# Performance work log

Hardware: AMD Instinct MI355X
Metric: run time of the kernel (lower is better)

Reference implementation:

```python
import jax, jax.numpy as jnp
import numpy as np

N_CTX = 4096
D_MODEL = 2048


def setup_inputs() -> dict:
    key = jax.random.key(0)
    k1, k2, k3 = jax.random.split(key, 3)
    embedding = jax.random.normal(k1, (N_CTX, D_MODEL), dtype=jnp.float32)
    # torch.rand -> uniform [0, 1)
    qk = jax.random.uniform(k2, (D_MODEL, D_MODEL), dtype=jnp.float32)
    ov = jax.random.uniform(k3, (D_MODEL, D_MODEL), dtype=jnp.float32)
    return {"embedding": embedding, "qk": qk, "ov": ov}


def reference(embedding, qk, ov):
    n = embedding.shape[0]
    # scores[i, j] = e_i @ qk @ e_j  -> [N, N]
    scores = (embedding @ qk) @ embedding.T
    # strict upper triangle gets -inf (causal mask), matching triu(-inf, diag=1)
    causal_mask = jnp.triu(jnp.full((n, n), -jnp.inf, dtype=scores.dtype), k=1)
    scores = scores + causal_mask
    attn = jax.nn.softmax(scores, axis=-1)  # nn.Softmax() on 2D -> dim=1
    return (attn @ embedding) @ ov
```

## Files before the change

### kernel.cpp

```cpp
#include <hip/hip_runtime.h>
#include <hip/hip_bf16.h>

#define N_CTX 4096
#define DM    2048

typedef __attribute__((ext_vector_type(8))) short short8;
typedef __attribute__((ext_vector_type(4))) float f32x4;
typedef unsigned short ushort_t;

__device__ __forceinline__ ushort_t f2bf(float x) {
    __hip_bfloat16 h = __float2bfloat16(x);
    return __builtin_bit_cast(ushort_t, h);
}
__device__ __forceinline__ float bf2f(ushort_t u) {
    return __bfloat162float(__builtin_bit_cast(__hip_bfloat16, u));
}

__device__ __forceinline__ void gload16(const void* g, void* l) {
    __builtin_amdgcn_global_load_lds((const __attribute__((address_space(1))) void*)g,
                                     (__attribute__((address_space(3))) void*)l,
                                     16, 0, 0);
}


__global__ __launch_bounds__(256) void split_cast_kernel(
    const float* __restrict__ in, ushort_t* __restrict__ hi, ushort_t* __restrict__ lo, int n4)
{
    int idx = blockIdx.x * 256 + threadIdx.x;
    if (idx >= n4) return;
    float4 v = reinterpret_cast<const float4*>(in)[idx];
    float vv[4] = {v.x, v.y, v.z, v.w};
    ushort_t h[4], l[4];
#pragma unroll
    for (int j = 0; j < 4; ++j) {
        h[j] = f2bf(vv[j]);
        l[j] = f2bf(vv[j] - bf2f(h[j]));
    }
    reinterpret_cast<ushort4*>(hi)[idx] = *reinterpret_cast<ushort4*>(h);
    reinterpret_cast<ushort4*>(lo)[idx] = *reinterpret_cast<ushort4*>(l);
}

template <bool SPLIT>
__global__ __launch_bounds__(256) void transpose_cast_kernel(
    const float* __restrict__ in, ushort_t* __restrict__ hi, ushort_t* __restrict__ lo,
    int R, int C)
{
    __shared__ float tile[32][33];
    int bc = blockIdx.x * 32;
    int br = blockIdx.y * 32;
    int tx = threadIdx.x, ty = threadIdx.y;
#pragma unroll
    for (int r = ty; r < 32; r += 8)
        tile[r][tx] = in[(size_t)(br + r) * C + bc + tx];
    __syncthreads();
#pragma unroll
    for (int c = ty; c < 32; c += 8) {
        float v = tile[tx][c];
        size_t o = (size_t)(bc + c) * R + br + tx;
        ushort_t h = f2bf(v);
        hi[o] = h;
        if (SPLIT) lo[o] = f2bf(v - bf2f(h));
    }
}


template <int NP, int OM, bool CAUSAL>
__global__ __launch_bounds__(256, 2) void gemm_bt_kernel(
    const ushort_t* __restrict__ A0, const ushort_t* __restrict__ B0,
    const ushort_t* __restrict__ A1, const ushort_t* __restrict__ B1,
    const ushort_t* __restrict__ A2, const ushort_t* __restrict__ B2,
    int K, int ldc,
    float* __restrict__ Cf, ushort_t* __restrict__ Ch, ushort_t* __restrict__ Cl)
{
    const int bx = blockIdx.x;
    const int by = blockIdx.y;
    if (CAUSAL && bx * 128 > by * 128 + 127) return;

    __shared__ ushort_t Asm[128 * 64];
    __shared__ ushort_t Bsm[128 * 64];

    const int t = threadIdx.x;
    const int l = t & 63;
    const int w = t >> 6;
    const int wr = w >> 1;
    const int wc = w & 1;

    f32x4 zero = {0.f, 0.f, 0.f, 0.f};
    f32x4 acc[4][4];
#pragma unroll
    for (int m = 0; m < 4; ++m)
#pragma unroll
        for (int n = 0; n < 4; ++n) acc[m][n] = zero;

    const size_t arow0 = (size_t)by * 128;
    const size_t brow0 = (size_t)bx * 128;

    const ushort_t* Aps[3] = {A0, A1, A2};
    const ushort_t* Bps[3] = {B0, B1, B2};

#pragma unroll
    for (int pt = 0; pt < NP; ++pt) {
        const ushort_t* Ap = Aps[pt];
        const ushort_t* Bp = Bps[pt];
        for (int kt = 0; kt < K; kt += 64) {
            __syncthreads();
#pragma unroll
            for (int i = 0; i < 4; ++i) {
                int f = i * 256 + t;
                int r = f >> 3;
                int cch = (f & 7) ^ (r & 7);
                const ushort_t* ga = Ap + (arow0 + r) * (size_t)K + kt + cch * 8;
                gload16(ga, (char*)Asm + (i * 256 + w * 64) * 16);
                const ushort_t* gb = Bp + (brow0 + r) * (size_t)K + kt + cch * 8;
                gload16(gb, (char*)Bsm + (i * 256 + w * 64) * 16);
            }
            __syncthreads();

#pragma unroll
            for (int kk = 0; kk < 2; ++kk) {
                short8 af[4], bfr[4];
#pragma unroll
                for (int m = 0; m < 4; ++m) {
                    int row = wr * 64 + m * 16 + (l & 15);
                    int gby = kk * 64 + (l >> 4) * 16;
                    af[m] = *(const short8*)((const char*)Asm + row * 128 +
                                             (gby ^ ((row & 7) * 16)));
                }
#pragma unroll
                for (int n = 0; n < 4; ++n) {
                    int row = wc * 64 + n * 16 + (l & 15);
                    int gby = kk * 64 + (l >> 4) * 16;
                    bfr[n] = *(const short8*)((const char*)Bsm + row * 128 +
                                              (gby ^ ((row & 7) * 16)));
                }
#pragma unroll
                for (int m = 0; m < 4; ++m)
#pragma unroll
                    for (int n = 0; n < 4; ++n)
                        acc[m][n] = __builtin_amdgcn_mfma_f32_16x16x32_bf16(
                            af[m], bfr[n], acc[m][n], 0, 0, 0);
            }
        }
    }

    const int r0 = by * 128 + wr * 64 + ((l >> 4) << 2);
    const int c0 = bx * 128 + wc * 64 + (l & 15);
#pragma unroll
    for (int m = 0; m < 4; ++m) {
#pragma unroll
        for (int n = 0; n < 4; ++n) {
#pragma unroll
            for (int j = 0; j < 4; ++j) {
                size_t o = (size_t)(r0 + m * 16 + j) * ldc + (c0 + n * 16);
                float v = acc[m][n][j];
                if (OM == 0) {
                    Cf[o] = v;
                } else if (OM == 1) {
                    Ch[o] = f2bf(v);
                } else {
                    ushort_t h = f2bf(v);
                    Ch[o] = h;
                    Cl[o] = f2bf(v - bf2f(h));
                }
            }
        }
    }
}


__device__ __forceinline__ float waveMax(float v) {
#pragma unroll
    for (int o = 32; o > 0; o >>= 1) v = fmaxf(v, __shfl_xor(v, o, 64));
    return v;
}
__device__ __forceinline__ float waveSum(float v) {
#pragma unroll
    for (int o = 32; o > 0; o >>= 1) v += __shfl_xor(v, o, 64);
    return v;
}

__global__ __launch_bounds__(256) void softmax_kernel(
    const float* __restrict__ S, ushort_t* __restrict__ A)
{
    const int i = blockIdx.x;
    __shared__ float row[N_CTX];
    __shared__ float red[8];
    const int t = threadIdx.x;
    const int len = i + 1;
    const float* Srow = S + (size_t)i * N_CTX;

    float m = -3.4e38f;
    for (int j = t; j < len; j += 256) {
        float v = Srow[j];
        row[j] = v;
        m = fmaxf(m, v);
    }
    m = waveMax(m);
    if ((t & 63) == 0) red[t >> 6] = m;
    __syncthreads();
    m = fmaxf(fmaxf(red[0], red[1]), fmaxf(red[2], red[3]));

    float s = 0.f;
    for (int j = t; j < len; j += 256) {
        float e = __expf(row[j] - m);
        row[j] = e;
        s += e;
    }
    s = waveSum(s);
    __syncthreads();
    if ((t & 63) == 0) red[t >> 6] = s;
    __syncthreads();
    float inv = 1.f / (red[0] + red[1] + red[2] + red[3]);

    ushort_t* Arow = A + (size_t)i * N_CTX;
    for (int j = t; j < N_CTX; j += 256)
        Arow[j] = (j < len) ? f2bf(row[j] * inv) : (ushort_t)0;
}


extern "C" void kernel_launch(void* const* d_in, const int* in_sizes, int n_in,
                              void* d_out, int out_size, void* d_ws, size_t ws_size,
                              hipStream_t stream)
{
    const float* E  = (const float*)d_in[0];
    const float* qk = (const float*)d_in[1];
    const float* ov = (const float*)d_in[2];
    float* out = (float*)d_out;

    char* ws = (char*)d_ws;
    size_t off = 0;
    auto take = [&](size_t bytes) -> char* {
        char* p = ws + off;
        off += (bytes + 255) & ~(size_t)255;
        return p;
    };

    ushort_t* Ehi   = (ushort_t*)take((size_t)N_CTX * DM * 2);
    ushort_t* Elo   = (ushort_t*)take((size_t)N_CTX * DM * 2);
    ushort_t* Et    = (ushort_t*)take((size_t)N_CTX * DM * 2);
    ushort_t* QKthi = (ushort_t*)take((size_t)DM * DM * 2);
    ushort_t* QKtlo = (ushort_t*)take((size_t)DM * DM * 2);
    ushort_t* OVt   = (ushort_t*)take((size_t)DM * DM * 2);
    ushort_t* Qhi   = (ushort_t*)take((size_t)N_CTX * DM * 2);
    ushort_t* Qlo   = (ushort_t*)take((size_t)N_CTX * DM * 2);
    float*    S     = (float*)take((size_t)N_CTX * N_CTX * 4);
    ushort_t* Attn  = (ushort_t*)take((size_t)N_CTX * N_CTX * 2);
    ushort_t* Hbf   = (ushort_t*)take((size_t)N_CTX * DM * 2);
    (void)ws_size; (void)in_sizes; (void)n_in; (void)out_size;

    split_cast_kernel<<<dim3((N_CTX * DM / 4) / 256), 256, 0, stream>>>(E, Ehi, Elo, N_CTX * DM / 4);
    transpose_cast_kernel<true ><<<dim3(DM / 32, DM / 32),    dim3(32, 8), 0, stream>>>(qk, QKthi, QKtlo, DM, DM);
    transpose_cast_kernel<false><<<dim3(DM / 32, DM / 32),    dim3(32, 8), 0, stream>>>(ov, OVt, nullptr, DM, DM);
    transpose_cast_kernel<false><<<dim3(DM / 32, N_CTX / 32), dim3(32, 8), 0, stream>>>(E, Et, nullptr, N_CTX, DM);

    gemm_bt_kernel<3, 2, false><<<dim3(DM / 128, N_CTX / 128), 256, 0, stream>>>(
        Ehi, QKthi, Ehi, QKtlo, Elo, QKthi, DM, DM, nullptr, Qhi, Qlo);

    gemm_bt_kernel<3, 0, true><<<dim3(N_CTX / 128, N_CTX / 128), 256, 0, stream>>>(
        Qhi, Ehi, Qhi, Elo, Qlo, Ehi, DM, N_CTX, S, nullptr, nullptr);

    softmax_kernel<<<N_CTX, 256, 0, stream>>>(S, Attn);

    gemm_bt_kernel<1, 1, false><<<dim3(DM / 128, N_CTX / 128), 256, 0, stream>>>(
        Attn, Et, nullptr, nullptr, nullptr, nullptr, N_CTX, DM, nullptr, Hbf, nullptr);

    gemm_bt_kernel<1, 0, false><<<dim3(DM / 128, N_CTX / 128), 256, 0, stream>>>(
        Hbf, OVt, nullptr, nullptr, nullptr, nullptr, DM, DM, out, nullptr, nullptr);
}
```

Measured before the change: 506.7 us.

## Rewrite GEMM as 8-wave 256x128 double-buffered pipelined kernel with causal K-limit

```diff
diff --git a/kernel.cpp b/kernel.cpp
--- a/kernel.cpp
+++ b/kernel.cpp
@@ -7,6 +7,9 @@
 typedef __attribute__((ext_vector_type(8))) short short8;
 typedef __attribute__((ext_vector_type(4))) float f32x4;
 typedef unsigned short ushort_t;
+
+#define SBAR() __builtin_amdgcn_sched_barrier(0)
+#define WBAR() __builtin_amdgcn_s_barrier()
 
 __device__ __forceinline__ ushort_t f2bf(float x) {
     __hip_bfloat16 h = __float2bfloat16(x);
@@ -64,91 +67,141 @@
 }
 
 
-template <int NP, int OM, bool CAUSAL>
-__global__ __launch_bounds__(256, 2) void gemm_bt_kernel(
+template <int NP, int OM, bool CAUSAL, bool CKLIM>
+__global__ __launch_bounds__(512, 2) void gemm8_kernel(
     const ushort_t* __restrict__ A0, const ushort_t* __restrict__ B0,
     const ushort_t* __restrict__ A1, const ushort_t* __restrict__ B1,
     const ushort_t* __restrict__ A2, const ushort_t* __restrict__ B2,
-    int K, int ldc,
+    int K, int kshift, int nbxs, int ldc,
     float* __restrict__ Cf, ushort_t* __restrict__ Ch, ushort_t* __restrict__ Cl)
 {
-    const int bx = blockIdx.x;
-    const int by = blockIdx.y;
-    if (CAUSAL && bx * 128 > by * 128 + 127) return;
-
-    __shared__ ushort_t Asm[128 * 64];
-    __shared__ ushort_t Bsm[128 * 64];
+    extern __shared__ char lds[];
+
+    const int nwg = gridDim.x;
+    const int q8 = nwg >> 3;
+    const int wgid = (blockIdx.x & 7) * q8 + (blockIdx.x >> 3);
+    const int by = wgid >> nbxs;
+    const int bx = wgid & ((1 << nbxs) - 1);
+    if (CAUSAL && bx * 128 > by * 256 + 255) return;
 
     const int t = threadIdx.x;
     const int l = t & 63;
     const int w = t >> 6;
     const int wr = w >> 1;
     const int wc = w & 1;
-
-    f32x4 zero = {0.f, 0.f, 0.f, 0.f};
+    const int lr = l & 15;
+    const int lc = l >> 4;
+
+    const size_t arow0 = (size_t)by * 256;
+    const size_t brow0 = (size_t)bx * 128;
+
+    int ntiles = (NP * K) >> 6;
+    if (CKLIM) { int lim = (by + 1) * 4; if (lim < ntiles) ntiles = lim; }
+    const int kmask = (K >> 6) - 1;
+
     f32x4 acc[4][4];
 #pragma unroll
     for (int m = 0; m < 4; ++m)
 #pragma unroll
-        for (int n = 0; n < 4; ++n) acc[m][n] = zero;
-
-    const size_t arow0 = (size_t)by * 128;
-    const size_t brow0 = (size_t)bx * 128;
-
-    const ushort_t* Aps[3] = {A0, A1, A2};
-    const ushort_t* Bps[3] = {B0, B1, B2};
-
-#pragma unroll
-    for (int pt = 0; pt < NP; ++pt) {
-        const ushort_t* Ap = Aps[pt];
-        const ushort_t* Bp = Bps[pt];
-        for (int kt = 0; kt < K; kt += 64) {
-            __syncthreads();
-#pragma unroll
-            for (int i = 0; i < 4; ++i) {
-                int f = i * 256 + t;
-                int r = f >> 3;
-                int cch = (f & 7) ^ (r & 7);
-                const ushort_t* ga = Ap + (arow0 + r) * (size_t)K + kt + cch * 8;
-                gload16(ga, (char*)Asm + (i * 256 + w * 64) * 16);
-                const ushort_t* gb = Bp + (brow0 + r) * (size_t)K + kt + cch * 8;
-                gload16(gb, (char*)Bsm + (i * 256 + w * 64) * 16);
+        for (int n = 0; n < 4; ++n) acc[m][n] = (f32x4){0.f, 0.f, 0.f, 0.f};
+
+    auto stage = [&](int T, int buf) {
+        int p = (NP > 1) ? (T >> kshift) : 0;
+        int kt = (T & kmask) << 6;
+        const ushort_t* Ap = A0; const ushort_t* Bp = B0;
+        if (NP > 1 && p == 1) { Ap = A1; Bp = B1; }
+        if (NP > 2 && p == 2) { Ap = A2; Bp = B2; }
+        char* ab = lds + buf * 32768;
+#pragma unroll
+        for (int i = 0; i < 4; ++i) {
+            int f = i * 512 + t;
+            int row = f >> 3, c = f & 7;
+            gload16(Ap + (arow0 + row) * (size_t)K + kt + ((c ^ (row & 7)) << 3),
+                    ab + f * 16);
+        }
+        char* bb = lds + 65536 + buf * 16384;
+#pragma unroll
+        for (int i = 0; i < 2; ++i) {
+            int f = i * 512 + t;
+            int row = f >> 3, c = f & 7;
+            gload16(Bp + (brow0 + row) * (size_t)K + kt + ((c ^ (row & 7)) << 3),
+                    bb + f * 16);
+        }
+    };
+
+    auto rdA = [&](short8* d, int mb, int buf) {
+        const char* base = lds + buf * 32768;
+#pragma unroll
+        for (int mi = 0; mi < 2; ++mi)
+#pragma unroll
+            for (int kk = 0; kk < 2; ++kk) {
+                int row = wr * 64 + (mb + mi) * 16 + lr;
+                d[mi * 2 + kk] = *(const short8*)(base + row * 128 +
+                                  ((((kk << 2) + lc) ^ (lr & 7)) << 4));
             }
-            __syncthreads();
-
+    };
+    auto rdB = [&](short8* d, int nb, int buf) {
+        const char* base = lds + 65536 + buf * 16384;
+#pragma unroll
+        for (int ni = 0; ni < 2; ++ni)
 #pragma unroll
             for (int kk = 0; kk < 2; ++kk) {
-                short8 af[4], bfr[4];
-#pragma unroll
-                for (int m = 0; m < 4; ++m) {
-                    int row = wr * 64 + m * 16 + (l & 15);
-                    int gby = kk * 64 + (l >> 4) * 16;
-                    af[m] = *(const short8*)((const char*)Asm + row * 128 +
-                                             (gby ^ ((row & 7) * 16)));
-                }
-#pragma unroll
-                for (int n = 0; n < 4; ++n) {
-                    int row = wc * 64 + n * 16 + (l & 15);
-                    int gby = kk * 64 + (l >> 4) * 16;
-                    bfr[n] = *(const short8*)((const char*)Bsm + row * 128 +
-                                              (gby ^ ((row & 7) * 16)));
-                }
-#pragma unroll
-                for (int m = 0; m < 4; ++m)
-#pragma unroll
-                    for (int n = 0; n < 4; ++n)
-                        acc[m][n] = __builtin_amdgcn_mfma_f32_16x16x32_bf16(
-                            af[m], bfr[n], acc[m][n], 0, 0, 0);
+                int row = wc * 64 + (nb + ni) * 16 + lr;
+                d[ni * 2 + kk] = *(const short8*)(base + row * 128 +
+                                  ((((kk << 2) + lc) ^ (lr & 7)) << 4));
             }
+    };
+    auto mm8 = [&](const short8* a, const short8* b, int mb, int nb) {
+#pragma unroll
+        for (int mi = 0; mi < 2; ++mi)
+#pragma unroll
+            for (int ni = 0; ni < 2; ++ni)
+#pragma unroll
+                for (int kk = 0; kk < 2; ++kk)
+                    acc[mb + mi][nb + ni] = __builtin_amdgcn_mfma_f32_16x16x32_bf16(
+                        a[mi * 2 + kk], b[ni * 2 + kk], acc[mb + mi][nb + ni], 0, 0, 0);
+    };
+
+    stage(0, 0);
+    stage(ntiles > 1 ? 1 : 0, 1);
+    asm volatile("s_waitcnt vmcnt(6)" ::: "memory");
+    SBAR(); WBAR(); SBAR();
+
+    const int nit = ntiles >> 1;
+    for (int it = 0; it < nit; ++it) {
+        int T2 = 2 * it + 2; if (T2 > ntiles - 1) T2 = ntiles - 1;
+        int T3 = 2 * it + 3; if (T3 > ntiles - 1) T3 = ntiles - 1;
+#pragma unroll
+        for (int h = 0; h < 2; ++h) {
+            const int buf = h;
+            const int Tp = h ? T3 : T2;
+            short8 a01[4], a23[4], b01[4], b23[4];
+            rdA(a01, 0, buf); rdB(b01, 0, buf);
+            SBAR(); WBAR(); SBAR();
+            __builtin_amdgcn_s_setprio(1); mm8(a01, b01, 0, 0); __builtin_amdgcn_s_setprio(0);
+            SBAR(); WBAR(); SBAR();
+            rdB(b23, 2, buf);
+            SBAR(); WBAR(); SBAR();
+            __builtin_amdgcn_s_setprio(1); mm8(a01, b23, 0, 2); __builtin_amdgcn_s_setprio(0);
+            SBAR(); WBAR(); SBAR();
+            rdA(a23, 2, buf);
+            SBAR(); WBAR(); SBAR();
+            __builtin_amdgcn_s_setprio(1); mm8(a23, b23, 2, 2); __builtin_amdgcn_s_setprio(0);
+            SBAR(); WBAR(); SBAR();
+            stage(Tp, buf);
+            asm volatile("s_waitcnt vmcnt(6)" ::: "memory");
+            SBAR(); WBAR(); SBAR();
+            __builtin_amdgcn_s_setprio(1); mm8(a23, b01, 2, 0); __builtin_amdgcn_s_setprio(0);
+            SBAR(); WBAR(); SBAR();
         }
     }
 
-    const int r0 = by * 128 + wr * 64 + ((l >> 4) << 2);
-    const int c0 = bx * 128 + wc * 64 + (l & 15);
-#pragma unroll
-    for (int m = 0; m < 4; ++m) {
-#pragma unroll
-        for (int n = 0; n < 4; ++n) {
+    const int r0 = by * 256 + wr * 64 + (lc << 2);
+    const int c0 = bx * 128 + wc * 64 + lr;
+#pragma unroll
+    for (int m = 0; m < 4; ++m)
+#pragma unroll
+        for (int n = 0; n < 4; ++n)
 #pragma unroll
             for (int j = 0; j < 4; ++j) {
                 size_t o = (size_t)(r0 + m * 16 + j) * ldc + (c0 + n * 16);
@@ -158,13 +211,11 @@
                 } else if (OM == 1) {
                     Ch[o] = f2bf(v);
                 } else {
-                    ushort_t h = f2bf(v);
-                    Ch[o] = h;
-                    Cl[o] = f2bf(v - bf2f(h));
+                    ushort_t hh = f2bf(v);
+                    Ch[o] = hh;
+                    Cl[o] = f2bf(v - bf2f(hh));
                 }
             }
-        }
-    }
 }
 
 
@@ -248,22 +299,32 @@
     ushort_t* Hbf   = (ushort_t*)take((size_t)N_CTX * DM * 2);
     (void)ws_size; (void)in_sizes; (void)n_in; (void)out_size;
 
+    constexpr int SMEM = 96 * 1024;
+    hipFuncSetAttribute((const void*)&gemm8_kernel<3, 2, false, false>,
+                        hipFuncAttributeMaxDynamicSharedMemorySize, SMEM);
+    hipFuncSetAttribute((const void*)&gemm8_kernel<3, 0, true, false>,
+                        hipFuncAttributeMaxDynamicSharedMemorySize, SMEM);
+    hipFuncSetAttribute((const void*)&gemm8_kernel<1, 1, false, true>,
+                        hipFuncAttributeMaxDynamicSharedMemorySize, SMEM);
+    hipFuncSetAttribute((const void*)&gemm8_kernel<1, 0, false, false>,
+                        hipFuncAttributeMaxDynamicSharedMemorySize, SMEM);
+
     split_cast_kernel<<<dim3((N_CTX * DM / 4) / 256), 256, 0, stream>>>(E, Ehi, Elo, N_CTX * DM / 4);
     transpose_cast_kernel<true ><<<dim3(DM / 32, DM / 32),    dim3(32, 8), 0, stream>>>(qk, QKthi, QKtlo, DM, DM);
     transpose_cast_kernel<false><<<dim3(DM / 32, DM / 32),    dim3(32, 8), 0, stream>>>(ov, OVt, nullptr, DM, DM);
     transpose_cast_kernel<false><<<dim3(DM / 32, N_CTX / 32), dim3(32, 8), 0, stream>>>(E, Et, nullptr, N_CTX, DM);
 
-    gemm_bt_kernel<3, 2, false><<<dim3(DM / 128, N_CTX / 128), 256, 0, stream>>>(
-        Ehi, QKthi, Ehi, QKtlo, Elo, QKthi, DM, DM, nullptr, Qhi, Qlo);
-
-    gemm_bt_kernel<3, 0, true><<<dim3(N_CTX / 128, N_CTX / 128), 256, 0, stream>>>(
-        Qhi, Ehi, Qhi, Elo, Qlo, Ehi, DM, N_CTX, S, nullptr, nullptr);
+    gemm8_kernel<3, 2, false, false><<<256, 512, SMEM, stream>>>(
+        Ehi, QKthi, Ehi, QKtlo, Elo, QKthi, DM, 5, 4, DM, nullptr, Qhi, Qlo);
+
+    gemm8_kernel<3, 0, true, false><<<512, 512, SMEM, stream>>>(
+        Qhi, Ehi, Qhi, Elo, Qlo, Ehi, DM, 5, 5, N_CTX, S, nullptr, nullptr);
 
     softmax_kernel<<<N_CTX, 256, 0, stream>>>(S, Attn);
 
-    gemm_bt_kernel<1, 1, false><<<dim3(DM / 128, N_CTX / 128), 256, 0, stream>>>(
-        Attn, Et, nullptr, nullptr, nullptr, nullptr, N_CTX, DM, nullptr, Hbf, nullptr);
-
-    gemm_bt_kernel<1, 0, false><<<dim3(DM / 128, N_CTX / 128), 256, 0, stream>>>(
-        Hbf, OVt, nullptr, nullptr, nullptr, nullptr, DM, DM, out, nullptr, nullptr);
-}
+    gemm8_kernel<1, 1, false, true><<<256, 512, SMEM, stream>>>(
+        Attn, Et, nullptr, nullptr, nullptr, nullptr, N_CTX, 6, 4, DM, nullptr, Hbf, nullptr);
+
+    gemm8_kernel<1, 0, false, false><<<256, 512, SMEM, stream>>>(
+        Hbf, OVt, nullptr, nullptr, nullptr, nullptr, DM, 5, 4, DM, out, nullptr, nullptr);
+}
```

Measured after the change: 1.377 ms. +171.7%, slower.

## Fuse split-bf16 GEMM passes into one K loop and skip causal-zero K range

Applied to the files above, without the earlier changes.

```diff
diff --git a/kernel.cpp b/kernel.cpp
--- a/kernel.cpp
+++ b/kernel.cpp
@@ -64,11 +64,10 @@
 }
 
 
-template <int NP, int OM, bool CAUSAL>
-__global__ __launch_bounds__(256, 2) void gemm_bt_kernel(
-    const ushort_t* __restrict__ A0, const ushort_t* __restrict__ B0,
-    const ushort_t* __restrict__ A1, const ushort_t* __restrict__ B1,
-    const ushort_t* __restrict__ A2, const ushort_t* __restrict__ B2,
+template <int OM, bool CAUSAL>
+__global__ __launch_bounds__(256, 2) void gemm_split_kernel(
+    const ushort_t* __restrict__ Ah, const ushort_t* __restrict__ Al,
+    const ushort_t* __restrict__ Bh, const ushort_t* __restrict__ Bl,
     int K, int ldc,
     float* __restrict__ Cf, ushort_t* __restrict__ Ch, ushort_t* __restrict__ Cl)
 {
@@ -76,8 +75,10 @@
     const int by = blockIdx.y;
     if (CAUSAL && bx * 128 > by * 128 + 127) return;
 
-    __shared__ ushort_t Asm[128 * 64];
-    __shared__ ushort_t Bsm[128 * 64];
+    __shared__ ushort_t AHs[128 * 64];
+    __shared__ ushort_t ALs[128 * 64];
+    __shared__ ushort_t BHs[128 * 64];
+    __shared__ ushort_t BLs[128 * 64];
 
     const int t = threadIdx.x;
     const int l = t & 63;
@@ -85,86 +86,167 @@
     const int wr = w >> 1;
     const int wc = w & 1;
 
-    f32x4 zero = {0.f, 0.f, 0.f, 0.f};
     f32x4 acc[4][4];
 #pragma unroll
     for (int m = 0; m < 4; ++m)
 #pragma unroll
-        for (int n = 0; n < 4; ++n) acc[m][n] = zero;
+        for (int n = 0; n < 4; ++n) acc[m][n] = (f32x4){0.f, 0.f, 0.f, 0.f};
 
     const size_t arow0 = (size_t)by * 128;
     const size_t brow0 = (size_t)bx * 128;
 
-    const ushort_t* Aps[3] = {A0, A1, A2};
-    const ushort_t* Bps[3] = {B0, B1, B2};
-
-#pragma unroll
-    for (int pt = 0; pt < NP; ++pt) {
-        const ushort_t* Ap = Aps[pt];
-        const ushort_t* Bp = Bps[pt];
-        for (int kt = 0; kt < K; kt += 64) {
-            __syncthreads();
-#pragma unroll
-            for (int i = 0; i < 4; ++i) {
-                int f = i * 256 + t;
-                int r = f >> 3;
-                int cch = (f & 7) ^ (r & 7);
-                const ushort_t* ga = Ap + (arow0 + r) * (size_t)K + kt + cch * 8;
-                gload16(ga, (char*)Asm + (i * 256 + w * 64) * 16);
-                const ushort_t* gb = Bp + (brow0 + r) * (size_t)K + kt + cch * 8;
-                gload16(gb, (char*)Bsm + (i * 256 + w * 64) * 16);
-            }
-            __syncthreads();
-
-#pragma unroll
-            for (int kk = 0; kk < 2; ++kk) {
-                short8 af[4], bfr[4];
-#pragma unroll
-                for (int m = 0; m < 4; ++m) {
-                    int row = wr * 64 + m * 16 + (l & 15);
-                    int gby = kk * 64 + (l >> 4) * 16;
-                    af[m] = *(const short8*)((const char*)Asm + row * 128 +
-                                             (gby ^ ((row & 7) * 16)));
-                }
-#pragma unroll
-                for (int n = 0; n < 4; ++n) {
-                    int row = wc * 64 + n * 16 + (l & 15);
-                    int gby = kk * 64 + (l >> 4) * 16;
-                    bfr[n] = *(const short8*)((const char*)Bsm + row * 128 +
-                                              (gby ^ ((row & 7) * 16)));
-                }
-#pragma unroll
-                for (int m = 0; m < 4; ++m)
-#pragma unroll
-                    for (int n = 0; n < 4; ++n)
-                        acc[m][n] = __builtin_amdgcn_mfma_f32_16x16x32_bf16(
-                            af[m], bfr[n], acc[m][n], 0, 0, 0);
-            }
+    auto stage1 = [&](const ushort_t* src, ushort_t* dst, size_t row0, int kt) {
+#pragma unroll
+        for (int i = 0; i < 4; ++i) {
+            int f = i * 256 + t;
+            int r = f >> 3;
+            int cch = (f & 7) ^ (r & 7);
+            gload16(src + (row0 + r) * (size_t)K + kt + cch * 8,
+                    (char*)dst + (i * 256 + w * 64) * 16);
+        }
+    };
+    auto rdf = [&](short8* d, const ushort_t* base, int rbase, int kk) {
+#pragma unroll
+        for (int m = 0; m < 4; ++m) {
+            int row = rbase + m * 16 + (l & 15);
+            int gby = kk * 64 + (l >> 4) * 16;
+            d[m] = *(const short8*)((const char*)base + row * 128 +
+                                    (gby ^ ((row & 7) * 16)));
+        }
+    };
+    auto mm16 = [&](const short8* a, const short8* b) {
+#pragma unroll
+        for (int m = 0; m < 4; ++m)
+#pragma unroll
+            for (int n = 0; n < 4; ++n)
+                acc[m][n] = __builtin_amdgcn_mfma_f32_16x16x32_bf16(
+                    a[m], b[n], acc[m][n], 0, 0, 0);
+    };
+
+    for (int kt = 0; kt < K; kt += 64) {
+        __syncthreads();
+        stage1(Ah, AHs, arow0, kt);
+        stage1(Al, ALs, arow0, kt);
+        stage1(Bh, BHs, brow0, kt);
+        stage1(Bl, BLs, brow0, kt);
+        __syncthreads();
+
+#pragma unroll
+        for (int kk = 0; kk < 2; ++kk) {
+            short8 ah[4], bh[4], x[4];
+            rdf(ah, AHs, wr * 64, kk);
+            rdf(bh, BHs, wc * 64, kk);
+            mm16(ah, bh);
+            rdf(x, BLs, wc * 64, kk);
+            mm16(ah, x);
+            rdf(x, ALs, wr * 64, kk);
+            mm16(x, bh);
         }
     }
 
     const int r0 = by * 128 + wr * 64 + ((l >> 4) << 2);
     const int c0 = bx * 128 + wc * 64 + (l & 15);
 #pragma unroll
-    for (int m = 0; m < 4; ++m) {
-#pragma unroll
-        for (int n = 0; n < 4; ++n) {
+    for (int m = 0; m < 4; ++m)
+#pragma unroll
+        for (int n = 0; n < 4; ++n)
 #pragma unroll
             for (int j = 0; j < 4; ++j) {
                 size_t o = (size_t)(r0 + m * 16 + j) * ldc + (c0 + n * 16);
                 float v = acc[m][n][j];
                 if (OM == 0) {
                     Cf[o] = v;
-                } else if (OM == 1) {
-                    Ch[o] = f2bf(v);
                 } else {
-                    ushort_t h = f2bf(v);
-                    Ch[o] = h;
-                    Cl[o] = f2bf(v - bf2f(h));
+                    ushort_t hh = f2bf(v);
+                    Ch[o] = hh;
+                    Cl[o] = f2bf(v - bf2f(hh));
                 }
             }
-        }
-    }
+}
+
+
+template <int OM, bool CKLIM>
+__global__ __launch_bounds__(256, 2) void gemm_bt_kernel(
+    const ushort_t* __restrict__ A, const ushort_t* __restrict__ B,
+    int K, int ldc,
+    float* __restrict__ Cf, ushort_t* __restrict__ Ch)
+{
+    const int bx = blockIdx.x;
+    const int by = blockIdx.y;
+
+    __shared__ ushort_t Asm[128 * 64];
+    __shared__ ushort_t Bsm[128 * 64];
+
+    const int t = threadIdx.x;
+    const int l = t & 63;
+    const int w = t >> 6;
+    const int wr = w >> 1;
+    const int wc = w & 1;
+
+    f32x4 acc[4][4];
+#pragma unroll
+    for (int m = 0; m < 4; ++m)
+#pragma unroll
+        for (int n = 0; n < 4; ++n) acc[m][n] = (f32x4){0.f, 0.f, 0.f, 0.f};
+
+    const size_t arow0 = (size_t)by * 128;
+    const size_t brow0 = (size_t)bx * 128;
+
+    int kend = K;
+    if (CKLIM) { int lim = (by + 1) * 128; if (lim < kend) kend = lim; }
+
+    for (int kt = 0; kt < kend; kt += 64) {
+        __syncthreads();
+#pragma unroll
+        for (int i = 0; i < 4; ++i) {
+            int f = i * 256 + t;
+            int r = f >> 3;
+            int cch = (f & 7) ^ (r & 7);
+            gload16(A + (arow0 + r) * (size_t)K + kt + cch * 8,
+                    (char*)Asm + (i * 256 + w * 64) * 16);
+            gload16(B + (brow0 + r) * (size_t)K + kt + cch * 8,
+                    (char*)Bsm + (i * 256 + w * 64) * 16);
+        }
+        __syncthreads();
+
+#pragma unroll
+        for (int kk = 0; kk < 2; ++kk) {
+            short8 af[4], bfr[4];
+#pragma unroll
+            for (int m = 0; m < 4; ++m) {
+                int row = wr * 64 + m * 16 + (l & 15);
+                int gby = kk * 64 + (l >> 4) * 16;
+                af[m] = *(const short8*)((const char*)Asm + row * 128 +
+                                         (gby ^ ((row & 7) * 16)));
+            }
+#pragma unroll
+            for (int n = 0; n < 4; ++n) {
+                int row = wc * 64 + n * 16 + (l & 15);
+                int gby = kk * 64 + (l >> 4) * 16;
+                bfr[n] = *(const short8*)((const char*)Bsm + row * 128 +
+                                          (gby ^ ((row & 7) * 16)));
+            }
+#pragma unroll
+            for (int m = 0; m < 4; ++m)
+#pragma unroll
+                for (int n = 0; n < 4; ++n)
+                    acc[m][n] = __builtin_amdgcn_mfma_f32_16x16x32_bf16(
+                        af[m], bfr[n], acc[m][n], 0, 0, 0);
+        }
+    }
+
+    const int r0 = by * 128 + wr * 64 + ((l >> 4) << 2);
+    const int c0 = bx * 128 + wc * 64 + (l & 15);
+#pragma unroll
+    for (int m = 0; m < 4; ++m)
+#pragma unroll
+        for (int n = 0; n < 4; ++n)
+#pragma unroll
+            for (int j = 0; j < 4; ++j) {
+                size_t o = (size_t)(r0 + m * 16 + j) * ldc + (c0 + n * 16);
+                if (OM == 0) Cf[o] = acc[m][n][j];
+                else         Ch[o] = f2bf(acc[m][n][j]);
+            }
 }
 
 
@@ -253,17 +335,17 @@
     transpose_cast_kernel<false><<<dim3(DM / 32, DM / 32),    dim3(32, 8), 0, stream>>>(ov, OVt, nullptr, DM, DM);
     transpose_cast_kernel<false><<<dim3(DM / 32, N_CTX / 32), dim3(32, 8), 0, stream>>>(E, Et, nullptr, N_CTX, DM);
 
-    gemm_bt_kernel<3, 2, false><<<dim3(DM / 128, N_CTX / 128), 256, 0, stream>>>(
-        Ehi, QKthi, Ehi, QKtlo, Elo, QKthi, DM, DM, nullptr, Qhi, Qlo);
-
-    gemm_bt_kernel<3, 0, true><<<dim3(N_CTX / 128, N_CTX / 128), 256, 0, stream>>>(
-        Qhi, Ehi, Qhi, Elo, Qlo, Ehi, DM, N_CTX, S, nullptr, nullptr);
+    gemm_split_kernel<2, false><<<dim3(DM / 128, N_CTX / 128), 256, 0, stream>>>(
+        Ehi, Elo, QKthi, QKtlo, DM, DM, nullptr, Qhi, Qlo);
+
+    gemm_split_kernel<0, true><<<dim3(N_CTX / 128, N_CTX / 128), 256, 0, stream>>>(
+        Qhi, Qlo, Ehi, Elo, DM, N_CTX, S, nullptr, nullptr);
 
     softmax_kernel<<<N_CTX, 256, 0, stream>>>(S, Attn);
 
-    gemm_bt_kernel<1, 1, false><<<dim3(DM / 128, N_CTX / 128), 256, 0, stream>>>(
-        Attn, Et, nullptr, nullptr, nullptr, nullptr, N_CTX, DM, nullptr, Hbf, nullptr);
-
-    gemm_bt_kernel<1, 0, false><<<dim3(DM / 128, N_CTX / 128), 256, 0, stream>>>(
-        Hbf, OVt, nullptr, nullptr, nullptr, nullptr, DM, DM, out, nullptr, nullptr);
-}
+    gemm_bt_kernel<1, true><<<dim3(DM / 128, N_CTX / 128), 256, 0, stream>>>(
+        Attn, Et, N_CTX, DM, nullptr, Hbf);
+
+    gemm_bt_kernel<0, false><<<dim3(DM / 128, N_CTX / 128), 256, 0, stream>>>(
+        Hbf, OVt, DM, DM, out, nullptr);
+}
```

Measured after the change: 469.0 us. 7.4% less time.
